# Kernel tuning notes

Measured on AMD Instinct MI355X. Metric: run time of the kernel, lower is better.

Reference implementation:

```python
import jax, jax.numpy as jnp
import numpy as np
from jax import lax

B, CIN, S = 16, 1, 64          # batch, input channels, spatial
C = 16                          # c_out hidden channels
T = 50                          # ODE steps
DT = 0.5
NC = 7                          # n_classes
K = T // 2 + 1                  # rfft bins = 26
HID = 256


def conv2d_same(x, w, b):
    # x:(B,Ci,H,W) w:(Co,Ci,3,3) zero 'SAME' padding (torch padding=1)
    y = lax.conv_general_dilated(x, w, (1, 1), 'SAME',
                                 dimension_numbers=('NCHW', 'OIHW', 'NCHW'))
    return y + b[None, :, None, None]


def conv2d_circular(x, w):
    # circular padding=1, no bias (coRNNCell.Wy)
    xp = jnp.pad(x, ((0, 0), (0, 0), (1, 1), (1, 1)), mode='wrap')
    return lax.conv_general_dilated(xp, w, (1, 1), 'VALID',
                                    dimension_numbers=('NCHW', 'OIHW', 'NCHW'))


def setup_inputs() -> dict:
    key = jax.random.key(0)
    ks = iter(jax.random.split(key, 40))
    d = {}
    d['x'] = jax.random.normal(next(ks), (B, CIN, S, S), dtype=jnp.float32)

    def cw(ci, co):
        return jax.random.normal(next(ks), (co, ci, 3, 3), jnp.float32) * (1.0 / np.sqrt(ci * 9))

    # omega / alpha encoders: 3 convs each
    for p in ('om', 'al'):
        d[f'{p}_w1'], d[f'{p}_b1'] = cw(CIN, C), jnp.zeros((C,), jnp.float32)
        d[f'{p}_w2'], d[f'{p}_b2'] = cw(C, C), jnp.zeros((C,), jnp.float32)
        d[f'{p}_w3'], d[f'{p}_b3'] = cw(C, C), jnp.zeros((C,), jnp.float32)
    # hy encoder: 4 convs
    d['hy_w1'], d['hy_b1'] = cw(CIN, C), jnp.zeros((C,), jnp.float32)
    d['hy_w2'], d['hy_b2'] = cw(C, C), jnp.zeros((C,), jnp.float32)
    d['hy_w3'], d['hy_b3'] = cw(C, C), jnp.zeros((C,), jnp.float32)
    d['hy_w4'], d['hy_b4'] = cw(C, C), jnp.zeros((C,), jnp.float32)
    # cell conv: block-diagonal discrete Laplacian (per torch init)
    lap = np.array([[0., 1., 0.], [1., -4., 1.], [0., 1., 0.]], np.float32)
    wy = np.zeros((C, C, 3, 3), np.float32)
    wy[np.arange(C), np.arange(C)] = lap
    d['wy'] = jnp.asarray(wy)
    # readout MLP: 416 -> 256 -> 256 -> 256 -> 7
    dims = [K * C, HID, HID, HID, NC]
    for i in range(4):
        d[f'ro_w{i+1}'] = jax.random.normal(next(ks), (dims[i], dims[i + 1]), jnp.float32) * (1.0 / np.sqrt(dims[i]))
        d[f'ro_b{i+1}'] = jnp.zeros((dims[i + 1],), jnp.float32)
    return d


def _forward(x,
             om_w1, om_b1, om_w2, om_b2, om_w3, om_b3,
             al_w1, al_b1, al_w2, al_b2, al_w3, al_b3,
             hy_w1, hy_b1, hy_w2, hy_b2, hy_w3, hy_b3, hy_w4, hy_b4,
             wy,
             ro_w1, ro_b1, ro_w2, ro_b2, ro_w3, ro_b3, ro_w4, ro_b4):
    relu = jax.nn.relu
    # encoders
    om = relu(conv2d_same(relu(conv2d_same(relu(conv2d_same(x, om_w1, om_b1)), om_w2, om_b2)), om_w3, om_b3))
    al = relu(conv2d_same(relu(conv2d_same(relu(conv2d_same(x, al_w1, al_b1)), al_w2, al_b2)), al_w3, al_b3))
    h = relu(conv2d_same(x, hy_w1, hy_b1))
    h = relu(conv2d_same(h, hy_w2, hy_b2))
    h = relu(conv2d_same(h, hy_w3, hy_b3))
    hy0 = jnp.tanh(conv2d_same(h, hy_w4, hy_b4))

    omega = om.reshape(B, C, S * S)
    alpha = al.reshape(B, C, S * S)
    hy = hy0.reshape(B, C, S * S)
    hz = jnp.zeros_like(hy)

    def step(carry, _):
        hy, hz = carry
        sf = jnp.tanh(conv2d_circular(hy.reshape(B, C, S, S), wy)).reshape(B, C, S * S)
        new_hz = hz + DT * (sf - omega * hy - alpha * hz)
        new_hy = hy + DT * new_hz
        return (new_hy, new_hz), new_hy

    _, y_seq = lax.scan(step, (hy, hz), None, length=T)   # (T,B,C,HW)
    y_seq = jnp.transpose(y_seq, (1, 3, 2, 0)).reshape(B * S * S, C, T)  # (BHW,C,T)

    fft_mag = jnp.abs(jnp.fft.rfft(y_seq, axis=2))        # (BHW,C,K)
    f = fft_mag.reshape(B * S * S, C * K)                  # (BHW, C*K)

    f = relu(f @ ro_w1 + ro_b1)
    f = relu(f @ ro_w2 + ro_b2)
    f = relu(f @ ro_w3 + ro_b3)
    logits_flat = f @ ro_w4 + ro_b4                        # (BHW, NC)
    logits = logits_flat.reshape(B, S, S, NC).transpose(0, 3, 1, 2)
    return logits


def reference(x,
              om_w1, om_b1, om_w2, om_b2, om_w3, om_b3,
              al_w1, al_b1, al_w2, al_b2, al_w3, al_b3,
              hy_w1, hy_b1, hy_w2, hy_b2, hy_w3, hy_b3, hy_w4, hy_b4,
              wy,
              ro_w1, ro_b1, ro_w2, ro_b2, ro_w3, ro_b3, ro_w4, ro_b4):
    return _forward(x,
                    om_w1, om_b1, om_w2, om_b2, om_w3, om_b3,
                    al_w1, al_b1, al_w2, al_b2, al_w3, al_b3,
                    hy_w1, hy_b1, hy_w2, hy_b2, hy_w3, hy_b3, hy_w4, hy_b4,
                    wy,
                    ro_w1, ro_b1, ro_w2, ro_b2, ro_w3, ro_b3, ro_w4, ro_b4)
```

## Files before the change

kernel.cpp:

```cpp
#include <hip/hip_runtime.h>
#include <hip/hip_bf16.h>
#include <hip/hip_fp16.h>
#include <math.h>

#define B_   16
#define C_   16
#define S_   64
#define HW_  4096
#define T_   50
#define K_   26
#define F_   416
#define HID_ 256
#define NC_  7
#define DT_  0.5f
#define BCHW_ (B_*C_*HW_)
#define M_   (B_*HW_)

typedef _Float16 f16x8  __attribute__((ext_vector_type(8)));
typedef __fp16   fp16x2 __attribute__((ext_vector_type(2)));
typedef float    f32x4  __attribute__((ext_vector_type(4)));
typedef float    f32x2  __attribute__((ext_vector_type(2)));

__device__ __forceinline__ void gld_lds16(const void* g, void* l){
    __builtin_amdgcn_global_load_lds(
        (const __attribute__((address_space(1))) void*)g,
        (__attribute__((address_space(3))) void*)l, 16, 0, 0);
}

__device__ __forceinline__ float fast_tanh(float x){
    float ax = fabsf(x);
    float e  = __expf(2.f*ax);
    float r  = 1.f - 2.f/(e + 1.f);
    return copysignf(r, x);
}

__device__ __forceinline__ short f2h_s(float f){
    __half h = __float2half(f);
    return *(short*)&h;
}

template<int CIN, int ACT>
__global__ __launch_bounds__(512) void convf_kernel(
    const float* __restrict__ in0, const float* __restrict__ in1, const float* __restrict__ in2,
    const float* __restrict__ w0,  const float* __restrict__ w1,  const float* __restrict__ w2,
    const float* __restrict__ b0,  const float* __restrict__ b1,  const float* __restrict__ b2,
    float* __restrict__ o0, float* __restrict__ o1, float* __restrict__ o2)
{
    __shared__ __align__(16) float slab[CIN][10][66];
    const int slice = blockIdx.x;
    const int b     = blockIdx.y;
    const int ch    = blockIdx.z;
    const float* in = (ch == 0) ? in0 : (ch == 1) ? in1 : in2;
    const float* w  = (ch == 0) ? w0  : (ch == 1) ? w1  : w2;
    const float* bb = (ch == 0) ? b0  : (ch == 1) ? b1  : b2;
    float* out      = (ch == 0) ? o0  : (ch == 1) ? o1  : o2;

    const int tid = threadIdx.x;
    const int y0  = slice * 8;

    for (int idx = tid; idx < CIN*10*66; idx += 512){
        int ci  = idx / (10*66);
        int rem = idx % (10*66);
        int rr  = rem / 66;
        int cc  = rem % 66;
        int gy = y0 - 1 + rr;
        int gx = cc - 1;
        float v = 0.f;
        if ((unsigned)gy < 64u && (unsigned)gx < 64u)
            v = in[(size_t)(b*CIN + ci)*HW_ + gy*64 + gx];
        slab[ci][rr][cc] = v;
    }
    __syncthreads();

    const int x  = tid & 63;
    const int ry = tid >> 6;

    float acc[16];
    #pragma unroll
    for (int co = 0; co < 16; co++) acc[co] = bb[co];

    for (int ci = 0; ci < CIN; ci++){
        float p[3][3];
        #pragma unroll
        for (int dy = 0; dy < 3; dy++)
            #pragma unroll
            for (int dx = 0; dx < 3; dx++)
                p[dy][dx] = slab[ci][ry + dy][x + dx];
        #pragma unroll
        for (int co = 0; co < 16; co++){
            const float* wp = w + (size_t)(co*CIN + ci)*9;
            float s = acc[co];
            #pragma unroll
            for (int dy = 0; dy < 3; dy++)
                #pragma unroll
                for (int dx = 0; dx < 3; dx++)
                    s = fmaf(wp[dy*3 + dx], p[dy][dx], s);
            acc[co] = s;
        }
    }
    #pragma unroll
    for (int co = 0; co < 16; co++){
        float v = acc[co];
        v = ACT ? fast_tanh(v) : fmaxf(v, 0.f);
        out[(size_t)(b*16 + co)*HW_ + (y0 + ry)*64 + x] = v;
    }
}

__global__ __launch_bounds__(1024) void ode_kernel(
    const float* __restrict__ omega, const float* __restrict__ alpha,
    const float* __restrict__ hy0,   const float* __restrict__ wy,
    __half* __restrict__ yseq)
{
    __shared__ __align__(16) float buf[2][64*68];
    const int blk = blockIdx.x;
    const int c   = blk & 15;
    const int tid = threadIdx.x;
    const int y   = tid >> 4;
    const int xq  = (tid & 15) << 2;
    const size_t off = (size_t)blk * HW_;
    const int g0  = y*64 + xq;

    float4 om4 = *(const float4*)(omega + off + g0);
    float4 al4 = *(const float4*)(alpha + off + g0);
    float4 h4  = *(const float4*)(hy0   + off + g0);

    f32x2 om2[2] = { (f32x2){DT_*om4.x, DT_*om4.y}, (f32x2){DT_*om4.z, DT_*om4.w} };
    f32x2 al2[2] = { (f32x2){1.f - DT_*al4.x, 1.f - DT_*al4.y},
                     (f32x2){1.f - DT_*al4.z, 1.f - DT_*al4.w} };
    f32x2 hz2[2] = { (f32x2){0.f, 0.f}, (f32x2){0.f, 0.f} };
    float hv[4]  = { h4.x, h4.y, h4.z, h4.w };
    *(float4*)&buf[0][y*68 + xq] = h4;

    float wv[9];
    const float* wp = wy + (size_t)(c*C_ + c)*9;
    #pragma unroll
    for (int j = 0; j < 9; j++) wv[j] = wp[j];
    const bool five = (wv[0]==0.f) & (wv[2]==0.f) & (wv[6]==0.f) & (wv[8]==0.f);
    const f32x2 w1v = (f32x2){wv[1], wv[1]};
    const f32x2 w3v = (f32x2){wv[3], wv[3]};
    const f32x2 w4v = (f32x2){wv[4], wv[4]};
    const f32x2 w5v = (f32x2){wv[5], wv[5]};
    const f32x2 w7v = (f32x2){wv[7], wv[7]};
    const f32x2 dt2 = (f32x2){DT_, DT_};
    __syncthreads();

    const int ym = ((y + 63) & 63) * 68;
    const int yp = ((y + 1)  & 63) * 68;
    const int yo = y * 68;
    const int xm = (xq + 63) & 63;
    const int xp = (xq + 4)  & 63;
    const __half* ybase = yseq + off + g0;

    int cur = 0;
    for (int t = 0; t < T_; t++){
        const float* hp = buf[cur];
        float* hn = buf[cur ^ 1];
        float4 up4 = *(const float4*)&hp[ym + xq];
        float4 dn4 = *(const float4*)&hp[yp + xq];
        float lft = hp[yo + xm];
        float rgt = hp[yo + xp];

        float ny0, ny1, ny2, ny3;
        if (five){
            f32x2 u0 = (f32x2){up4.x, up4.y}, u1 = (f32x2){up4.z, up4.w};
            f32x2 d0 = (f32x2){dn4.x, dn4.y}, d1 = (f32x2){dn4.z, dn4.w};
            f32x2 c0 = (f32x2){hv[0], hv[1]}, c1 = (f32x2){hv[2], hv[3]};
            f32x2 l0 = (f32x2){lft,  hv[0]};
            f32x2 l1 = (f32x2){hv[1], hv[2]};
            f32x2 r1 = (f32x2){hv[3], rgt};

            f32x2 s0 = w4v*c0 + w1v*u0 + w7v*d0 + w3v*l0 + w5v*l1;
            f32x2 s1 = w4v*c1 + w1v*u1 + w7v*d1 + w3v*l1 + w5v*r1;

            f32x2 sf0 = (f32x2){fast_tanh(s0.x), fast_tanh(s0.y)};
            f32x2 sf1 = (f32x2){fast_tanh(s1.x), fast_tanh(s1.y)};

            f32x2 nz0 = al2[0]*hz2[0] - om2[0]*c0 + dt2*sf0;
            f32x2 nz1 = al2[1]*hz2[1] - om2[1]*c1 + dt2*sf1;
            f32x2 nyv0 = dt2*nz0 + c0;
            f32x2 nyv1 = dt2*nz1 + c1;
            hz2[0] = nz0; hz2[1] = nz1;
            ny0 = nyv0.x; ny1 = nyv0.y; ny2 = nyv1.x; ny3 = nyv1.y;
        } else {
            float upv[4] = {up4.x, up4.y, up4.z, up4.w};
            float dnv[4] = {dn4.x, dn4.y, dn4.z, dn4.w};
            float ul = hp[ym + xm], ur = hp[ym + xp];
            float dl = hp[yp + xm], dr = hp[yp + xp];
            float hzl[4] = {hz2[0].x, hz2[0].y, hz2[1].x, hz2[1].y};
            float oml[4] = {om2[0].x, om2[0].y, om2[1].x, om2[1].y};
            float all[4] = {al2[0].x, al2[0].y, al2[1].x, al2[1].y};
            float nyv[4];
            #pragma unroll
            for (int i = 0; i < 4; i++){
                float l  = (i == 0) ? lft : hv[i-1];
                float r  = (i == 3) ? rgt : hv[i+1];
                float uL = (i == 0) ? ul  : upv[i-1];
                float uR = (i == 3) ? ur  : upv[i+1];
                float dL = (i == 0) ? dl  : dnv[i-1];
                float dR = (i == 3) ? dr  : dnv[i+1];
                float s = wv[0]*uL + wv[1]*upv[i] + wv[2]*uR
                        + wv[3]*l  + wv[4]*hv[i]  + wv[5]*r
                        + wv[6]*dL + wv[7]*dnv[i] + wv[8]*dR;
                float sf = fast_tanh(s);
                float nz = fmaf(all[i], hzl[i], fmaf(-oml[i], hv[i], DT_*sf));
                nyv[i] = fmaf(DT_, nz, hv[i]);
                hzl[i] = nz;
            }
            hz2[0] = (f32x2){hzl[0], hzl[1]};
            hz2[1] = (f32x2){hzl[2], hzl[3]};
            ny0 = nyv[0]; ny1 = nyv[1]; ny2 = nyv[2]; ny3 = nyv[3];
        }

        hv[0] = ny0; hv[1] = ny1; hv[2] = ny2; hv[3] = ny3;
        *(float4*)&hn[yo + xq] = make_float4(ny0, ny1, ny2, ny3);

        union { fp16x2 h2[2]; uint2 u; } pk;
        pk.h2[0] = __builtin_amdgcn_cvt_pkrtz(ny0, ny1);
        pk.h2[1] = __builtin_amdgcn_cvt_pkrtz(ny2, ny3);
        *(uint2*)(ybase + (size_t)t*BCHW_) = pk.u;

        __syncthreads();
        cur ^= 1;
    }
}

__global__ __launch_bounds__(256) void dft_mfma_kernel(
    const __half* __restrict__ yseq, __half* __restrict__ f)
{
    __shared__ __align__(16) char Ys[8*256*16];
    __shared__ __align__(16) char Gs[8*64*16];
    const int tid = threadIdx.x;
    const int blk = blockIdx.x;
    const int bc  = blk >> 4;
    const int p0  = (blk & 15) << 8;
    const int b   = bc >> 4, c = bc & 15;

    for (int idx = tid; idx < 64*64; idx += 256){
        int r = idx >> 6, t = idx & 63;
        float v = 0.f;
        if (r < 52 && t < 50){
            int k  = r >> 1;
            int ph = (k * t) % 50;
            float ang = (float)ph * (6.2831853071795864f / 50.f);
            v = (r & 1) ? __sinf(ang) : __cosf(ang);
        }
        *(_Float16*)(Gs + ((t >> 3)*64 + r)*16 + (t & 7)*2) = (_Float16)v;
    }

    {
        const __half* src = yseq + (size_t)bc*HW_ + p0 + tid;
        #pragma unroll
        for (int t2 = 0; t2 < 25; t2++){
            unsigned int a = *(const unsigned short*)&src[(size_t)(2*t2)*BCHW_];
            unsigned int d = *(const unsigned short*)&src[(size_t)(2*t2+1)*BCHW_];
            int t8 = t2 >> 2, j = t2 & 3;
            *(unsigned int*)(Ys + (t8*256 + tid)*16 + j*4) = a | (d << 16);
        }
        #pragma unroll
        for (int t2 = 25; t2 < 32; t2++){
            int t8 = t2 >> 2, j = t2 & 3;
            *(unsigned int*)(Ys + (t8*256 + tid)*16 + j*4) = 0u;
        }
    }
    __syncthreads();

    const int lane = tid & 63;
    const int w    = tid >> 6;
    const int n    = lane & 15;
    const int quad = lane >> 4;
    const int mrow = 16*w + n;

    f16x8 a0 = *(const f16x8*)(Gs + ((quad    )*64 + mrow)*16);
    f16x8 a1 = *(const f16x8*)(Gs + ((quad + 4)*64 + mrow)*16);

    const int kb0   = 8*w + 2*quad;
    const bool valid = (kb0 < K_);

    for (int nt = 0; nt < 16; nt++){
        f16x8 b0 = *(const f16x8*)(Ys + ((quad    )*256 + nt*16 + n)*16);
        f16x8 b1 = *(const f16x8*)(Ys + ((quad + 4)*256 + nt*16 + n)*16);
        f32x4 acc = (f32x4){0.f, 0.f, 0.f, 0.f};
        acc = __builtin_amdgcn_mfma_f32_16x16x32_f16(a0, b0, acc, 0, 0, 0);
        acc = __builtin_amdgcn_mfma_f32_16x16x32_f16(a1, b1, acc, 0, 0, 0);
        if (valid){
            float m0 = sqrtf(fmaf(acc[0], acc[0], acc[1]*acc[1]));
            float m1 = sqrtf(fmaf(acc[2], acc[2], acc[3]*acc[3]));
            unsigned int u = ((unsigned int)(unsigned short)f2h_s(m1) << 16)
                           |  (unsigned int)(unsigned short)f2h_s(m0);
            const int row = b*HW_ + p0 + nt*16 + n;
            *(unsigned int*)((char*)(f + (size_t)row*F_ + c*K_) + kb0*2) = u;
        }
    }
}

__global__ __launch_bounds__(256) void prep_all_kernel(
    const float* __restrict__ w1, const float* __restrict__ w2,
    const float* __restrict__ w3,
    __half* __restrict__ wt1, __half* __restrict__ wt2, __half* __restrict__ wt3)
{
    const int blk = blockIdx.x;
    const int tid = threadIdx.x;
    if (blk < 256){
        const int n = blk;
        for (int k = tid; k < F_; k += 256)
            wt1[(size_t)n*F_ + k] = __float2half(w1[(size_t)k*HID_ + n]);
    } else if (blk < 512){
        const int n = blk - 256;
        for (int k = tid; k < HID_; k += 256)
            wt2[(size_t)n*HID_ + k] = __float2half(w2[(size_t)k*HID_ + n]);
    } else {
        const int n = blk - 512;
        for (int k = tid; k < HID_; k += 256)
            wt3[(size_t)n*HID_ + k] = __float2half(w3[(size_t)k*HID_ + n]);
    }
}

__global__ __launch_bounds__(512, 2) void mlp_fused_kernel(
    const __half* __restrict__ A,
    const __half* __restrict__ Wt1,
    const __half* __restrict__ Wt2,
    const __half* __restrict__ Wt3,
    const float* __restrict__ b1, const float* __restrict__ b2,
    const float* __restrict__ b3,
    const float* __restrict__ w4, const float* __restrict__ b4,
    float* __restrict__ out)
{
    __shared__ __align__(16) short hbuf[256*264];
    __shared__ __align__(16) short Bs[4*2064];
    __shared__ __align__(16) short Bs4[512*8];

    const int tid  = threadIdx.x;
    const int lane = tid & 63;
    const int wave = tid >> 6;
    const int wm   = (wave & 3) * 64;
    const int wn   = (wave >> 2) * 128;
    const int n16  = lane & 15;
    const int quad = lane >> 4;
    const int m0   = blockIdx.x * 256;

    {
        const int ktq = tid >> 4, n = tid & 15;
        short vals[8];
        #pragma unroll
        for (int e = 0; e < 8; e++){
            const int k = ktq*8 + e;
            vals[e] = f2h_s((n < NC_) ? w4[(size_t)k*NC_ + n] : 0.f);
        }
        #pragma unroll
        for (int e = 0; e < 8; e++) Bs4[tid*8 + e] = vals[e];
    }

    const int id0 = tid, id1 = tid + 512;
    const int kc0 = id0 >> 8, nn0 = id0 & 255;
    const int kc1 = id1 >> 8, nn1 = id1 & 255;
    char* dst0 = (char*)Bs + kc0*4128 + nn0*16;
    char* dst1 = (char*)Bs + kc1*4128 + nn1*16;

    f32x4 acc[4][8];
    #pragma unroll
    for (int i = 0; i < 4; i++)
        #pragma unroll
        for (int j = 0; j < 8; j++)
            acc[i][j] = (f32x4){0.f,0.f,0.f,0.f};

    const __half* arow[4];
    #pragma unroll
    for (int i = 0; i < 4; i++)
        arow[i] = A + (size_t)(m0 + wm + i*16 + n16)*F_ + quad*8;

    f16x8 afn[4];
    #pragma unroll
    for (int i = 0; i < 4; i++) afn[i] = *(const f16x8*)(arow[i]);

    for (int k0 = 0; k0 < F_; k0 += 32){
        gld_lds16(Wt1 + (size_t)nn0*F_ + k0 + kc0*8, dst0);
        gld_lds16(Wt1 + (size_t)nn1*F_ + k0 + kc1*8, dst1);
        __syncthreads();
        f16x8 af[4];
        #pragma unroll
        for (int i = 0; i < 4; i++) af[i] = afn[i];
        if (k0 + 32 < F_){
            #pragma unroll
            for (int i = 0; i < 4; i++) afn[i] = *(const f16x8*)(arow[i] + k0 + 32);
        }
        f16x8 bf[8];
        #pragma unroll
        for (int j = 0; j < 8; j++)
            bf[j] = *(const f16x8*)((char*)Bs + quad*4128 + (wn + j*16 + n16)*16);
        #pragma unroll
        for (int i = 0; i < 4; i++)
            #pragma unroll
            for (int j = 0; j < 8; j++)
                acc[i][j] = __builtin_amdgcn_mfma_f32_16x16x32_f16(
                                af[i], bf[j], acc[i][j], 0, 0, 0);
        __syncthreads();
    }
    #pragma unroll
    for (int j = 0; j < 8; j++){
        const int col = wn + j*16 + n16;
        const float bv = b1[col];
        #pragma unroll
        for (int i = 0; i < 4; i++){
            const int r0 = wm + i*16 + quad*4;
            #pragma unroll
            for (int r = 0; r < 4; r++)
                hbuf[(r0 + r)*264 + col] = f2h_s(fmaxf(acc[i][j][r] + bv, 0.f));
        }
    }
    __syncthreads();

    const __half* Wts[2] = {Wt2, Wt3};
    const float* bls[2] = {b2, b3};
    for (int L = 0; L < 2; L++){
        const __half* Wt = Wts[L];
        #pragma unroll
        for (int i = 0; i < 4; i++)
            #pragma unroll
            for (int j = 0; j < 8; j++)
                acc[i][j] = (f32x4){0.f,0.f,0.f,0.f};

        for (int k0 = 0; k0 < HID_; k0 += 32){
            gld_lds16(Wt + (size_t)nn0*HID_ + k0 + kc0*8, dst0);
            gld_lds16(Wt + (size_t)nn1*HID_ + k0 + kc1*8, dst1);
            f16x8 af[4];
            #pragma unroll
            for (int i = 0; i < 4; i++)
                af[i] = *(const f16x8*)&hbuf[(wm + i*16 + n16)*264 + k0 + quad*8];
            __syncthreads();
            f16x8 bf[8];
            #pragma unroll
            for (int j = 0; j < 8; j++)
                bf[j] = *(const f16x8*)((char*)Bs + quad*4128 + (wn + j*16 + n16)*16);
            #pragma unroll
            for (int i = 0; i < 4; i++)
                #pragma unroll
                for (int j = 0; j < 8; j++)
                    acc[i][j] = __builtin_amdgcn_mfma_f32_16x16x32_f16(
                                    af[i], bf[j], acc[i][j], 0, 0, 0);
            __syncthreads();
        }
        const float* bl = bls[L];
        #pragma unroll
        for (int j = 0; j < 8; j++){
            const int col = wn + j*16 + n16;
            const float bv = bl[col];
            #pragma unroll
            for (int i = 0; i < 4; i++){
                const int r0 = wm + i*16 + quad*4;
                #pragma unroll
                for (int r = 0; r < 4; r++)
                    hbuf[(r0 + r)*264 + col] = f2h_s(fmaxf(acc[i][j][r] + bv, 0.f));
            }
        }
        __syncthreads();
    }

    f32x4 facc[2] = {(f32x4){0.f,0.f,0.f,0.f}, (f32x4){0.f,0.f,0.f,0.f}};
    #pragma unroll
    for (int kt = 0; kt < 8; kt++){
        f16x8 bfr = *(const f16x8*)&Bs4[((kt*4 + quad)*16 + n16)*8];
        #pragma unroll
        for (int mt = 0; mt < 2; mt++){
            f16x8 af = *(const f16x8*)&hbuf[(wave*32 + mt*16 + n16)*264 + kt*32 + quad*8];
            facc[mt] = __builtin_amdgcn_mfma_f32_16x16x32_f16(af, bfr, facc[mt], 0, 0, 0);
        }
    }
    if (n16 < NC_){
        const float bv = b4[n16];
        #pragma unroll
        for (int mt = 0; mt < 2; mt++){
            #pragma unroll
            for (int r = 0; r < 4; r++){
                const int grow = m0 + wave*32 + mt*16 + quad*4 + r;
                const int bidx = grow >> 12, hw = grow & 4095;
                out[(size_t)(bidx*NC_ + n16)*HW_ + hw] = facc[mt][r] + bv;
            }
        }
    }
}

extern "C" void kernel_launch(void* const* d_in, const int* in_sizes, int n_in,
                              void* d_out, int out_size, void* d_ws, size_t ws_size,
                              hipStream_t stream)
{
    const float* x     = (const float*)d_in[0];
    const float* om_w1 = (const float*)d_in[1];  const float* om_b1 = (const float*)d_in[2];
    const float* om_w2 = (const float*)d_in[3];  const float* om_b2 = (const float*)d_in[4];
    const float* om_w3 = (const float*)d_in[5];  const float* om_b3 = (const float*)d_in[6];
    const float* al_w1 = (const float*)d_in[7];  const float* al_b1 = (const float*)d_in[8];
    const float* al_w2 = (const float*)d_in[9];  const float* al_b2 = (const float*)d_in[10];
    const float* al_w3 = (const float*)d_in[11]; const float* al_b3 = (const float*)d_in[12];
    const float* hy_w1 = (const float*)d_in[13]; const float* hy_b1 = (const float*)d_in[14];
    const float* hy_w2 = (const float*)d_in[15]; const float* hy_b2 = (const float*)d_in[16];
    const float* hy_w3 = (const float*)d_in[17]; const float* hy_b3 = (const float*)d_in[18];
    const float* hy_w4 = (const float*)d_in[19]; const float* hy_b4 = (const float*)d_in[20];
    const float* wy    = (const float*)d_in[21];
    const float* ro_w1 = (const float*)d_in[22]; const float* ro_b1 = (const float*)d_in[23];
    const float* ro_w2 = (const float*)d_in[24]; const float* ro_b2 = (const float*)d_in[25];
    const float* ro_w3 = (const float*)d_in[26]; const float* ro_b3 = (const float*)d_in[27];
    const float* ro_w4 = (const float*)d_in[28]; const float* ro_b4 = (const float*)d_in[29];
    float* out = (float*)d_out;

    char* wsb = (char*)d_ws;
    const size_t YSEQ_BYTES = (size_t)T_ * BCHW_ * 2;
    __half* yseq = (__half*)wsb;
    __half* fbuf = (__half*)(wsb + YSEQ_BYTES);

    const size_t MB4 = (size_t)BCHW_ * 4;
    float* om_t1 = (float*)(wsb + YSEQ_BYTES + 0*MB4);
    float* al_t1 = (float*)(wsb + YSEQ_BYTES + 1*MB4);
    float* hy_t1 = (float*)(wsb + YSEQ_BYTES + 2*MB4);
    float* om_t2 = (float*)(wsb + YSEQ_BYTES + 3*MB4);
    float* al_t2 = (float*)(wsb + YSEQ_BYTES + 4*MB4);
    float* hy_t2 = (float*)(wsb + YSEQ_BYTES + 5*MB4);
    float* omega = (float*)(wsb + YSEQ_BYTES + 6*MB4);
    float* alpha = (float*)(wsb + YSEQ_BYTES + 7*MB4);
    float* hy_t3 = (float*)(wsb + YSEQ_BYTES + 8*MB4);
    float* hy0   = (float*)(wsb + YSEQ_BYTES + 9*MB4);

    __half* wt1 = (__half*)(wsb + 0);
    __half* wt2 = (__half*)(wsb + 212992);
    __half* wt3 = (__half*)(wsb + 344064);

    convf_kernel<1,0><<<dim3(8,B_,3), 512, 0, stream>>>(
        x, x, x, om_w1, al_w1, hy_w1, om_b1, al_b1, hy_b1, om_t1, al_t1, hy_t1);
    convf_kernel<16,0><<<dim3(8,B_,3), 512, 0, stream>>>(
        om_t1, al_t1, hy_t1, om_w2, al_w2, hy_w2, om_b2, al_b2, hy_b2, om_t2, al_t2, hy_t2);
    convf_kernel<16,0><<<dim3(8,B_,3), 512, 0, stream>>>(
        om_t2, al_t2, hy_t2, om_w3, al_w3, hy_w3, om_b3, al_b3, hy_b3, omega, alpha, hy_t3);
    convf_kernel<16,1><<<dim3(8,B_,1), 512, 0, stream>>>(
        hy_t3, hy_t3, hy_t3, hy_w4, hy_w4, hy_w4, hy_b4, hy_b4, hy_b4, hy0, hy0, hy0);
    ode_kernel<<<256, 1024, 0, stream>>>(omega, alpha, hy0, wy, yseq);
    dft_mfma_kernel<<<4096, 256, 0, stream>>>(yseq, fbuf);
    prep_all_kernel<<<768, 256, 0, stream>>>(ro_w1, ro_w2, ro_w3, wt1, wt2, wt3);
    mlp_fused_kernel<<<256, 512, 0, stream>>>(
        fbuf, wt1, wt2, wt3, ro_b1, ro_b2, ro_b3, ro_w4, ro_b4, out);
}
```

Baseline: 372.5 us.

## Fuse encoder conv stack into one kernel with fp16 LDS intermediates

Replaces four separate conv launches with a single encoder kernel that computes all conv layers per 16-row slice, keeping intermediates in shared memory as fp16 and using halo recomputation. This removes global-memory round trips for intermediate activations and launch overheads. It adds halo recompute, reduces the grid to 192 blocks of 1024 threads, and stores intermediates in reduced precision.

```diff
diff --git a/kernel.cpp b/kernel.cpp
--- a/kernel.cpp
+++ b/kernel.cpp
@@ -39,70 +39,233 @@
     return *(short*)&h;
 }
 
-template<int CIN, int ACT>
-__global__ __launch_bounds__(512) void convf_kernel(
-    const float* __restrict__ in0, const float* __restrict__ in1, const float* __restrict__ in2,
-    const float* __restrict__ w0,  const float* __restrict__ w1,  const float* __restrict__ w2,
-    const float* __restrict__ b0,  const float* __restrict__ b1,  const float* __restrict__ b2,
-    float* __restrict__ o0, float* __restrict__ o1, float* __restrict__ o2)
+__device__ __forceinline__ void st2h(short* p, float a, float b){
+    union{ fp16x2 h; unsigned u; } q;
+    q.h = __builtin_amdgcn_cvt_pkrtz(a, b);
+    *(unsigned*)p = q.u;
+}
+__device__ __forceinline__ float h2f_lo(unsigned u){
+    unsigned short s = (unsigned short)u;
+    __half h = *(__half*)&s; return __half2float(h);
+}
+__device__ __forceinline__ float h2f_hi(unsigned u){
+    unsigned short s = (unsigned short)(u >> 16);
+    __half h = *(__half*)&s; return __half2float(h);
+}
+
+__global__ __launch_bounds__(1024) void encoder_kernel(
+    const float* __restrict__ x,
+    const float* __restrict__ w1a, const float* __restrict__ b1a,
+    const float* __restrict__ w2a, const float* __restrict__ b2a,
+    const float* __restrict__ w3a, const float* __restrict__ b3a,
+    const float* __restrict__ w1b, const float* __restrict__ b1b,
+    const float* __restrict__ w2b, const float* __restrict__ b2b,
+    const float* __restrict__ w3b, const float* __restrict__ b3b,
+    const float* __restrict__ w1c, const float* __restrict__ b1c,
+    const float* __restrict__ w2c, const float* __restrict__ b2c,
+    const float* __restrict__ w3c, const float* __restrict__ b3c,
+    const float* __restrict__ w4c, const float* __restrict__ b4c,
+    float* __restrict__ o_om, float* __restrict__ o_al, float* __restrict__ o_hy)
 {
-    __shared__ __align__(16) float slab[CIN][10][66];
+    __shared__ __align__(16) short As [16][22][68];
+    __shared__ __align__(16) short Bsl[16][20][68];
+
     const int slice = blockIdx.x;
     const int b     = blockIdx.y;
     const int ch    = blockIdx.z;
-    const float* in = (ch == 0) ? in0 : (ch == 1) ? in1 : in2;
-    const float* w  = (ch == 0) ? w0  : (ch == 1) ? w1  : w2;
-    const float* bb = (ch == 0) ? b0  : (ch == 1) ? b1  : b2;
-    float* out      = (ch == 0) ? o0  : (ch == 1) ? o1  : o2;
-
-    const int tid = threadIdx.x;
-    const int y0  = slice * 8;
-
-    for (int idx = tid; idx < CIN*10*66; idx += 512){
-        int ci  = idx / (10*66);
-        int rem = idx % (10*66);
-        int rr  = rem / 66;
-        int cc  = rem % 66;
-        int gy = y0 - 1 + rr;
-        int gx = cc - 1;
-        float v = 0.f;
-        if ((unsigned)gy < 64u && (unsigned)gx < 64u)
-            v = in[(size_t)(b*CIN + ci)*HW_ + gy*64 + gx];
-        slab[ci][rr][cc] = v;
+    const int tid   = threadIdx.x;
+    const int y0    = slice * 16;
+    const int nL    = (ch == 2) ? 4 : 3;
+
+    const float* W1 = (ch==0)?w1a:(ch==1)?w1b:w1c;
+    const float* Bi1= (ch==0)?b1a:(ch==1)?b1b:b1c;
+    const float* W2 = (ch==0)?w2a:(ch==1)?w2b:w2c;
+    const float* Bi2= (ch==0)?b2a:(ch==1)?b2b:b2c;
+    const float* W3 = (ch==0)?w3a:(ch==1)?w3b:w3c;
+    const float* Bi3= (ch==0)?b3a:(ch==1)?b3b:b3c;
+    float* outp = (ch==0)?o_om:(ch==1)?o_al:o_hy;
+
+    {
+        float* xs = (float*)Bsl;
+        const int rx = 16 + 2*nL;
+        for (int idx = tid; idx < rx*68; idx += 1024){
+            int row = idx / 68, col = idx % 68;
+            int g  = y0 - nL + row;
+            int gc = col - 2;
+            float v = 0.f;
+            if ((unsigned)g < 64u && (unsigned)gc < 64u)
+                v = x[(size_t)b*HW_ + g*64 + gc];
+            xs[row*68 + col] = v;
+        }
     }
     __syncthreads();
 
-    const int x  = tid & 63;
-    const int ry = tid >> 6;
-
-    float acc[16];
-    #pragma unroll
-    for (int co = 0; co < 16; co++) acc[co] = bb[co];
-
-    for (int ci = 0; ci < CIN; ci++){
-        float p[3][3];
-        #pragma unroll
-        for (int dy = 0; dy < 3; dy++)
-            #pragma unroll
-            for (int dx = 0; dx < 3; dx++)
-                p[dy][dx] = slab[ci][ry + dy][x + dx];
-        #pragma unroll
-        for (int co = 0; co < 16; co++){
-            const float* wp = w + (size_t)(co*CIN + ci)*9;
-            float s = acc[co];
-            #pragma unroll
-            for (int dy = 0; dy < 3; dy++)
-                #pragma unroll
-                for (int dx = 0; dx < 3; dx++)
-                    s = fmaf(wp[dy*3 + dx], p[dy][dx], s);
-            acc[co] = s;
-        }
-    }
-    #pragma unroll
-    for (int co = 0; co < 16; co++){
-        float v = acc[co];
-        v = ACT ? fast_tanh(v) : fmaxf(v, 0.f);
-        out[(size_t)(b*16 + co)*HW_ + (y0 + ry)*64 + x] = v;
+    {
+        const float* xs = (const float*)Bsl;
+        const int r1 = 16 + 2*(nL-1);
+        for (int slot = tid; slot < r1*32; slot += 1024){
+            const int row = slot >> 5;
+            const int x2  = (slot & 31) * 2;
+            const int g   = y0 - (nL-1) + row;
+            f32x2 acc[16];
+            #pragma unroll
+            for (int co = 0; co < 16; co++) acc[co] = (f32x2){Bi1[co], Bi1[co]};
+            #pragma unroll
+            for (int dy = 0; dy < 3; dy++){
+                const float* xr = &xs[(row+dy)*68 + x2 + 1];
+                float s0 = xr[0], s1 = xr[1], s2 = xr[2], s3 = xr[3];
+                f32x2 p0 = (f32x2){s0,s1}, p1 = (f32x2){s1,s2}, p2 = (f32x2){s2,s3};
+                #pragma unroll
+                for (int co = 0; co < 16; co++){
+                    const float* wp = W1 + co*9 + dy*3;
+                    acc[co] += (f32x2){wp[0],wp[0]}*p0
+                             + (f32x2){wp[1],wp[1]}*p1
+                             + (f32x2){wp[2],wp[2]}*p2;
+                }
+            }
+            const bool in = ((unsigned)g < 64u);
+            #pragma unroll
+            for (int co = 0; co < 16; co++){
+                float v0 = in ? fmaxf(acc[co].x, 0.f) : 0.f;
+                float v1 = in ? fmaxf(acc[co].y, 0.f) : 0.f;
+                st2h(&As[co][row][x2+2], v0, v1);
+                if (x2 == 0){ As[co][row][0] = 0; As[co][row][1] = 0; }
+                if (x2 == 62){ As[co][row][66] = 0; As[co][row][67] = 0; }
+            }
+        }
+    }
+    __syncthreads();
+
+    {
+        const int r2 = 16 + 2*(nL-2);
+        for (int slot = tid; slot < r2*32; slot += 1024){
+            const int row = slot >> 5;
+            const int x2  = (slot & 31) * 2;
+            const int g   = y0 - (nL-2) + row;
+            f32x2 acc[16];
+            #pragma unroll
+            for (int co = 0; co < 16; co++) acc[co] = (f32x2){Bi2[co], Bi2[co]};
+            #pragma unroll 1
+            for (int ci = 0; ci < 16; ci++){
+                #pragma unroll
+                for (int dy = 0; dy < 3; dy++){
+                    const short* ar = &As[ci][row+dy][x2];
+                    unsigned u0 = *(const unsigned*)(ar);
+                    unsigned u1 = *(const unsigned*)(ar+2);
+                    unsigned u2 = *(const unsigned*)(ar+4);
+                    float s0 = h2f_hi(u0), s1 = h2f_lo(u1);
+                    float s2 = h2f_hi(u1), s3 = h2f_lo(u2);
+                    f32x2 p0 = (f32x2){s0,s1}, p1 = (f32x2){s1,s2}, p2 = (f32x2){s2,s3};
+                    #pragma unroll
+                    for (int co = 0; co < 16; co++){
+                        const float* wp = W2 + (size_t)(co*16 + ci)*9 + dy*3;
+                        acc[co] += (f32x2){wp[0],wp[0]}*p0
+                                 + (f32x2){wp[1],wp[1]}*p1
+                                 + (f32x2){wp[2],wp[2]}*p2;
+                    }
+                }
+            }
+            const bool in = ((unsigned)g < 64u);
+            #pragma unroll
+            for (int co = 0; co < 16; co++){
+                float v0 = in ? fmaxf(acc[co].x, 0.f) : 0.f;
+                float v1 = in ? fmaxf(acc[co].y, 0.f) : 0.f;
+                st2h(&Bsl[co][row][x2+2], v0, v1);
+                if (x2 == 0){ Bsl[co][row][0] = 0; Bsl[co][row][1] = 0; }
+                if (x2 == 62){ Bsl[co][row][66] = 0; Bsl[co][row][67] = 0; }
+            }
+        }
+    }
+    __syncthreads();
+
+    {
+        const int r3 = 16 + 2*(nL-3);
+        for (int slot = tid; slot < r3*32; slot += 1024){
+            const int row = slot >> 5;
+            const int x2  = (slot & 31) * 2;
+            const int g   = y0 - (nL-3) + row;
+            f32x2 acc[16];
+            #pragma unroll
+            for (int co = 0; co < 16; co++) acc[co] = (f32x2){Bi3[co], Bi3[co]};
+            #pragma unroll 1
+            for (int ci = 0; ci < 16; ci++){
+                #pragma unroll
+                for (int dy = 0; dy < 3; dy++){
+                    const short* ar = &Bsl[ci][row+dy][x2];
+                    unsigned u0 = *(const unsigned*)(ar);
+                    unsigned u1 = *(const unsigned*)(ar+2);
+                    unsigned u2 = *(const unsigned*)(ar+4);
+                    float s0 = h2f_hi(u0), s1 = h2f_lo(u1);
+                    float s2 = h2f_hi(u1), s3 = h2f_lo(u2);
+                    f32x2 p0 = (f32x2){s0,s1}, p1 = (f32x2){s1,s2}, p2 = (f32x2){s2,s3};
+                    #pragma unroll
+                    for (int co = 0; co < 16; co++){
+                        const float* wp = W3 + (size_t)(co*16 + ci)*9 + dy*3;
+                        acc[co] += (f32x2){wp[0],wp[0]}*p0
+                                 + (f32x2){wp[1],wp[1]}*p1
+                                 + (f32x2){wp[2],wp[2]}*p2;
+                    }
+                }
+            }
+            if (ch != 2){
+                #pragma unroll
+                for (int co = 0; co < 16; co++){
+                    float v0 = fmaxf(acc[co].x, 0.f);
+                    float v1 = fmaxf(acc[co].y, 0.f);
+                    *(float2*)&outp[(size_t)(b*16 + co)*HW_ + g*64 + x2] =
+                        make_float2(v0, v1);
+                }
+            } else {
+                const bool in = ((unsigned)g < 64u);
+                #pragma unroll
+                for (int co = 0; co < 16; co++){
+                    float v0 = in ? fmaxf(acc[co].x, 0.f) : 0.f;
+                    float v1 = in ? fmaxf(acc[co].y, 0.f) : 0.f;
+                    st2h(&As[co][row][x2+2], v0, v1);
+                    if (x2 == 0){ As[co][row][0] = 0; As[co][row][1] = 0; }
+                    if (x2 == 62){ As[co][row][66] = 0; As[co][row][67] = 0; }
+                }
+            }
+        }
+    }
+
+    if (ch == 2){
+        __syncthreads();
+        for (int slot = tid; slot < 16*32; slot += 1024){
+            const int row = slot >> 5;
+            const int x2  = (slot & 31) * 2;
+            const int g   = y0 + row;
+            f32x2 acc[16];
+            #pragma unroll
+            for (int co = 0; co < 16; co++) acc[co] = (f32x2){b4c[co], b4c[co]};
+            #pragma unroll 1
+            for (int ci = 0; ci < 16; ci++){
+                #pragma unroll
+                for (int dy = 0; dy < 3; dy++){
+                    const short* ar = &As[ci][row+dy][x2];
+                    unsigned u0 = *(const unsigned*)(ar);
+                    unsigned u1 = *(const unsigned*)(ar+2);
+                    unsigned u2 = *(const unsigned*)(ar+4);
+                    float s0 = h2f_hi(u0), s1 = h2f_lo(u1);
+                    float s2 = h2f_hi(u1), s3 = h2f_lo(u2);
+                    f32x2 p0 = (f32x2){s0,s1}, p1 = (f32x2){s1,s2}, p2 = (f32x2){s2,s3};
+                    #pragma unroll
+                    for (int co = 0; co < 16; co++){
+                        const float* wp = w4c + (size_t)(co*16 + ci)*9 + dy*3;
+                        acc[co] += (f32x2){wp[0],wp[0]}*p0
+                                 + (f32x2){wp[1],wp[1]}*p1
+                                 + (f32x2){wp[2],wp[2]}*p2;
+                    }
+                }
+            }
+            #pragma unroll
+            for (int co = 0; co < 16; co++){
+                float v0 = fast_tanh(acc[co].x);
+                float v1 = fast_tanh(acc[co].y);
+                *(float2*)&outp[(size_t)(b*16 + co)*HW_ + g*64 + x2] =
+                    make_float2(v0, v1);
+            }
+        }
     }
 }
 
@@ -507,29 +670,20 @@
     __half* fbuf = (__half*)(wsb + YSEQ_BYTES);
 
     const size_t MB4 = (size_t)BCHW_ * 4;
-    float* om_t1 = (float*)(wsb + YSEQ_BYTES + 0*MB4);
-    float* al_t1 = (float*)(wsb + YSEQ_BYTES + 1*MB4);
-    float* hy_t1 = (float*)(wsb + YSEQ_BYTES + 2*MB4);
-    float* om_t2 = (float*)(wsb + YSEQ_BYTES + 3*MB4);
-    float* al_t2 = (float*)(wsb + YSEQ_BYTES + 4*MB4);
-    float* hy_t2 = (float*)(wsb + YSEQ_BYTES + 5*MB4);
-    float* omega = (float*)(wsb + YSEQ_BYTES + 6*MB4);
-    float* alpha = (float*)(wsb + YSEQ_BYTES + 7*MB4);
-    float* hy_t3 = (float*)(wsb + YSEQ_BYTES + 8*MB4);
-    float* hy0   = (float*)(wsb + YSEQ_BYTES + 9*MB4);
+    float* omega = (float*)(wsb + YSEQ_BYTES + 0*MB4);
+    float* alpha = (float*)(wsb + YSEQ_BYTES + 1*MB4);
+    float* hy0   = (float*)(wsb + YSEQ_BYTES + 2*MB4);
 
     __half* wt1 = (__half*)(wsb + 0);
     __half* wt2 = (__half*)(wsb + 212992);
     __half* wt3 = (__half*)(wsb + 344064);
 
-    convf_kernel<1,0><<<dim3(8,B_,3), 512, 0, stream>>>(
-        x, x, x, om_w1, al_w1, hy_w1, om_b1, al_b1, hy_b1, om_t1, al_t1, hy_t1);
-    convf_kernel<16,0><<<dim3(8,B_,3), 512, 0, stream>>>(
-        om_t1, al_t1, hy_t1, om_w2, al_w2, hy_w2, om_b2, al_b2, hy_b2, om_t2, al_t2, hy_t2);
-    convf_kernel<16,0><<<dim3(8,B_,3), 512, 0, stream>>>(
-        om_t2, al_t2, hy_t2, om_w3, al_w3, hy_w3, om_b3, al_b3, hy_b3, omega, alpha, hy_t3);
-    convf_kernel<16,1><<<dim3(8,B_,1), 512, 0, stream>>>(
-        hy_t3, hy_t3, hy_t3, hy_w4, hy_w4, hy_w4, hy_b4, hy_b4, hy_b4, hy0, hy0, hy0);
+    encoder_kernel<<<dim3(4, B_, 3), 1024, 0, stream>>>(
+        x,
+        om_w1, om_b1, om_w2, om_b2, om_w3, om_b3,
+        al_w1, al_b1, al_w2, al_b2, al_w3, al_b3,
+        hy_w1, hy_b1, hy_w2, hy_b2, hy_w3, hy_b3, hy_w4, hy_b4,
+        omega, alpha, hy0);
     ode_kernel<<<256, 1024, 0, stream>>>(omega, alpha, hy0, wy, yseq);
     dft_mfma_kernel<<<4096, 256, 0, stream>>>(yseq, fbuf);
     prep_all_kernel<<<768, 256, 0, stream>>>(ro_w1, ro_w2, ro_w3, wt1, wt2, wt3);
```

Result: slower. 435.8 us (+17.0%).
